# Kernel optimization log

Measured on AMD Instinct MI355X. Metric: run time of the kernel, lower is better.

## Reference

```python
import jax, jax.numpy as jnp
import numpy as np

N_HEAD = 16
N_STATE = 1024
D_HEAD = N_STATE // N_HEAD
B, T = 4, 2048


def setup_inputs() -> dict:
    key = jax.random.key(0)
    ks = jax.random.split(key, 9)
    x = jax.random.normal(ks[0], (B, T, N_STATE), dtype=jnp.float32)
    # causal additive mask, (T, T)
    neg = jnp.float32(-1e9)
    mask = jnp.where(jnp.tril(jnp.ones((T, T), dtype=bool)), 0.0, neg).astype(jnp.float32)
    s = 0.02  # keep activations in a sane range (module uses torch.randn init)
    Wq = jax.random.normal(ks[1], (N_STATE, N_STATE), dtype=jnp.float32) * s
    bq = jax.random.normal(ks[2], (N_STATE,), dtype=jnp.float32) * s
    Wk = jax.random.normal(ks[3], (N_STATE, N_STATE), dtype=jnp.float32) * s
    Wv = jax.random.normal(ks[4], (N_STATE, N_STATE), dtype=jnp.float32) * s
    bv = jax.random.normal(ks[5], (N_STATE,), dtype=jnp.float32) * s
    Wo = jax.random.normal(ks[6], (N_STATE, N_STATE), dtype=jnp.float32) * s
    bo = jax.random.normal(ks[7], (N_STATE,), dtype=jnp.float32) * s
    return {"x": x, "mask": mask, "Wq": Wq, "bq": bq, "Wk": Wk,
            "Wv": Wv, "bv": bv, "Wo": Wo, "bo": bo}


def reference(x, mask, Wq, bq, Wk, Wv, bv, Wo, bo):
    n, t, _ = x.shape
    scale = D_HEAD ** -0.25
    # projections: Linear stores weight as (out, in), applies x @ W.T
    q = x @ Wq.T + bq
    k = x @ Wk.T          # key has no bias
    v = x @ Wv.T + bv
    # (N, H, T, d)
    q = q.reshape(n, t, N_HEAD, D_HEAD).transpose(0, 2, 1, 3) * scale
    k = k.reshape(n, t, N_HEAD, D_HEAD).transpose(0, 2, 1, 3) * scale
    v = v.reshape(n, t, N_HEAD, D_HEAD).transpose(0, 2, 1, 3)
    qk = jnp.einsum('bhqd,bhkd->bhqk', q, k)
    qk = qk + mask[:t, :t]
    attn = jax.nn.softmax(qk, axis=-1)
    qkv = jnp.einsum('bhqk,bhkd->bhqd', attn, v)
    qkv = qkv.transpose(0, 2, 1, 3).reshape(n, t, N_STATE)
    return qkv @ Wo.T + bo
```

## Files before the change

kernel.cpp:

```cpp
#include <hip/hip_runtime.h>
#include <stdint.h>

#define DEVI __device__ __forceinline__

typedef float        f32x4   __attribute__((ext_vector_type(4)));
typedef float        f32x16  __attribute__((ext_vector_type(16)));
typedef __bf16       bf16x8  __attribute__((ext_vector_type(8)));
typedef unsigned short u16x8 __attribute__((ext_vector_type(8)));
typedef uint32_t     u32x2   __attribute__((ext_vector_type(2)));
typedef uint32_t     u32x4   __attribute__((ext_vector_type(4)));

static constexpr int TSEQ   = 2048;
static constexpr int NSTATE = 1024;
static constexpr int NHEAD  = 16;
static constexpr int DHEAD  = 64;
static constexpr int BATCH  = 4;
static constexpr int MROWS  = BATCH * TSEQ;
static constexpr float QSCALE = 0.125f * 1.44269504088896340736f;
static constexpr float DEFER_THR = 8.0f * 1.44269504088896340736f;

DEVI unsigned short f2bf(float f) {
  union { float f; uint32_t u; } v; v.f = f;
  return (unsigned short)((v.u + 0x7fffu + ((v.u >> 16) & 1u)) >> 16);
}

DEVI uint32_t cvt_pk_bf16(float lo, float hi) {
  uint32_t r;
  asm("v_cvt_pk_bf16_f32 %0, %1, %2" : "=v"(r) : "v"(lo), "v"(hi));
  return r;
}
DEVI float fexp2(float x) {
  float r;
  asm("v_exp_f32 %0, %1" : "=v"(r) : "v"(x));
  return r;
}

DEVI f32x4 mfma16(u16x8 a, u16x8 b, f32x4 c) {
  return __builtin_amdgcn_mfma_f32_16x16x32_bf16(
      __builtin_bit_cast(bf16x8, a), __builtin_bit_cast(bf16x8, b), c, 0, 0, 0);
}
DEVI f32x16 mfma32(u16x8 a, u16x8 b, f32x16 c) {
  return __builtin_amdgcn_mfma_f32_32x32x16_bf16(
      __builtin_bit_cast(bf16x8, a), __builtin_bit_cast(bf16x8, b), c, 0, 0, 0);
}

DEVI void gload_lds16(const void* g, void* l) {
  __builtin_amdgcn_global_load_lds(
      (const __attribute__((address_space(1))) void*)g,
      (__attribute__((address_space(3))) void*)l, 16, 0, 0);
}

__global__ void cvt_all(const float* __restrict__ x,
                        const float* __restrict__ w0, const float* __restrict__ w1,
                        const float* __restrict__ w2, const float* __restrict__ w3,
                        unsigned short* __restrict__ xb,
                        unsigned short* __restrict__ wb)
{
  const int NX = (MROWS * NSTATE) / 4;
  const int NW = (NSTATE * NSTATE) / 4;
  const int total = NX + 4 * NW;
  int i = blockIdx.x * blockDim.x + threadIdx.x;
  const int stride = gridDim.x * blockDim.x;
  for (; i < total; i += stride) {
    const float* src;
    unsigned short* dst;
    int j;
    if (i < NX) { src = x; dst = xb; j = i; }
    else {
      const int k = i - NX, wi = k >> 18;
      src = (wi == 0) ? w0 : (wi == 1) ? w1 : (wi == 2) ? w2 : w3;
      dst = wb + ((size_t)wi << 20);
      j = k & (NW - 1);
    }
    const float4 f = ((const float4*)src)[j];
    ushort4 o;
    o.x = f2bf(f.x); o.y = f2bf(f.y); o.z = f2bf(f.z); o.w = f2bf(f.w);
    ((ushort4*)dst)[j] = o;
  }
}

__global__ __launch_bounds__(256)
void gemm_qkv(const unsigned short* __restrict__ A,
              const unsigned short* __restrict__ Wqkv,
              const float* __restrict__ bq, const float* __restrict__ bv,
              unsigned short* __restrict__ Oqkv)
{
  __shared__ __align__(16) unsigned short As[128 * 32];
  __shared__ __align__(16) unsigned short Bs[128 * 32];
  const int t  = threadIdx.x;
  const int l  = t & 63, w = t >> 6;
  const int fr = l & 15, fq = l >> 4;
  const int wi = blockIdx.x >> 3;
  const int n0 = (blockIdx.x & 7) * 128;
  const int m0 = blockIdx.y * 128;
  const int wm = (w & 1) * 64, wn = (w >> 1) * 64;
  const unsigned short* Bw = Wqkv + ((size_t)wi << 20);
  unsigned short* Cq = Oqkv + ((size_t)wi << 23);

  f32x4 acc[4][4] = {};

  const int sr = t >> 2;
  const int sc = (t & 3) * 8;
  const unsigned short* ag = A  + (size_t)(m0 + sr) * NSTATE + sc;
  const unsigned short* bg = Bw + (size_t)(n0 + sr) * NSTATE + sc;
  unsigned short* lA0 = As + t * 8;
  unsigned short* lA1 = As + 2048 + t * 8;
  unsigned short* lB0 = Bs + t * 8;
  unsigned short* lB1 = Bs + 2048 + t * 8;

  for (int kt = 0; kt < NSTATE / 32; ++kt) {
    const int ko = kt * 32;
    gload_lds16(ag + ko,               lA0);
    gload_lds16(ag + 64 * NSTATE + ko, lA1);
    gload_lds16(bg + ko,               lB0);
    gload_lds16(bg + 64 * NSTATE + ko, lB1);
    __syncthreads();

    u16x8 a[4], b[4];
    #pragma unroll
    for (int i = 0; i < 4; ++i)
      a[i] = *(const u16x8*)(As + (wm + i * 16 + fr) * 32 + fq * 8);
    #pragma unroll
    for (int j = 0; j < 4; ++j)
      b[j] = *(const u16x8*)(Bs + (wn + j * 16 + fr) * 32 + fq * 8);
    #pragma unroll
    for (int i = 0; i < 4; ++i)
      #pragma unroll
      for (int j = 0; j < 4; ++j)
        acc[i][j] = mfma16(a[i], b[j], acc[i][j]);
    __syncthreads();
  }

  const int h = (n0 + wn) >> 6;
  #pragma unroll
  for (int j = 0; j < 4; ++j) {
    const int d = j * 16 + fr;
    const float bj = (wi == 1) ? 0.0f
                   : ((wi == 0) ? bq[n0 + wn + d] : bv[n0 + wn + d]);
    #pragma unroll
    for (int i = 0; i < 4; ++i) {
      #pragma unroll
      for (int r = 0; r < 4; ++r) {
        const int row = m0 + wm + i * 16 + fq * 4 + r;
        const int bb = row >> 11, tt = row & (TSEQ - 1);
        float v = acc[i][j][r] + bj;
        if (wi == 0) v *= QSCALE;
        Cq[(((size_t)(bb * NHEAD + h)) * TSEQ + tt) * DHEAD + d] = f2bf(v);
      }
    }
  }
}

__global__ __launch_bounds__(256)
void gemm_out(const unsigned short* __restrict__ A,
              const unsigned short* __restrict__ Bw,
              const float* __restrict__ bias,
              float* __restrict__ Co)
{
  __shared__ __align__(16) unsigned short As[128 * 32];
  __shared__ __align__(16) unsigned short Bs[128 * 32];
  const int t  = threadIdx.x;
  const int l  = t & 63, w = t >> 6;
  const int fr = l & 15, fq = l >> 4;
  const int m0 = blockIdx.y * 128, n0 = blockIdx.x * 128;
  const int wm = (w & 1) * 64, wn = (w >> 1) * 64;

  f32x4 acc[4][4] = {};

  const int sr = t >> 2;
  const int sc = (t & 3) * 8;
  const unsigned short* ag = A  + (size_t)(m0 + sr) * NSTATE + sc;
  const unsigned short* bg = Bw + (size_t)(n0 + sr) * NSTATE + sc;
  unsigned short* lA0 = As + t * 8;
  unsigned short* lA1 = As + 2048 + t * 8;
  unsigned short* lB0 = Bs + t * 8;
  unsigned short* lB1 = Bs + 2048 + t * 8;

  for (int kt = 0; kt < NSTATE / 32; ++kt) {
    const int ko = kt * 32;
    gload_lds16(ag + ko,               lA0);
    gload_lds16(ag + 64 * NSTATE + ko, lA1);
    gload_lds16(bg + ko,               lB0);
    gload_lds16(bg + 64 * NSTATE + ko, lB1);
    __syncthreads();

    u16x8 a[4], b[4];
    #pragma unroll
    for (int i = 0; i < 4; ++i)
      a[i] = *(const u16x8*)(As + (wm + i * 16 + fr) * 32 + fq * 8);
    #pragma unroll
    for (int j = 0; j < 4; ++j)
      b[j] = *(const u16x8*)(Bs + (wn + j * 16 + fr) * 32 + fq * 8);
    #pragma unroll
    for (int i = 0; i < 4; ++i)
      #pragma unroll
      for (int j = 0; j < 4; ++j)
        acc[i][j] = mfma16(a[i], b[j], acc[i][j]);
    __syncthreads();
  }

  #pragma unroll
  for (int j = 0; j < 4; ++j) {
    const int col = n0 + wn + j * 16 + fr;
    const float bj = bias[col];
    #pragma unroll
    for (int i = 0; i < 4; ++i) {
      const int row0 = m0 + wm + i * 16 + fq * 4;
      #pragma unroll
      for (int r = 0; r < 4; ++r)
        Co[(size_t)(row0 + r) * NSTATE + col] = acc[i][j][r] + bj;
    }
  }
}

__global__ __launch_bounds__(256)
void flash_attn(const unsigned short* __restrict__ Qg,
                const unsigned short* __restrict__ Kg,
                const unsigned short* __restrict__ Vg,
                unsigned short* __restrict__ O)
{
  const int bh = blockIdx.x;
  const int qb = 15 - (int)blockIdx.y;
  const int b  = bh >> 4, h = bh & 15;
  const int t  = threadIdx.x, lane = t & 63, w = t >> 6;
  const int lq = lane & 31, hi = lane >> 5;
  const size_t hoff = (size_t)bh * TSEQ * DHEAD;
  const unsigned short* Qp = Qg + hoff;
  const unsigned short* Kp = Kg + hoff;
  const unsigned short* Vp = Vg + hoff;

  __shared__ __align__(16) unsigned short Kb[2][64 * 64];
  __shared__ __align__(16) unsigned short Vb[2][64 * 64];

  const int qw   = qb * 128 + w * 32;
  const int qrow = qw + lq;

  u16x8 qf[4];
  #pragma unroll
  for (int c = 0; c < 4; ++c)
    qf[c] = *(const u16x8*)(Qp + (size_t)qrow * DHEAD + c * 16 + hi * 8);

  f32x16 oacc[2] = {};
  float m_r = -1e30f, l_r = 0.0f;

  const char* KbB = (const char*)&Kb[0][0];
  const char* VbB = (const char*)&Vb[0][0];
  int koff[4], voff[4];
  #pragma unroll
  for (int c = 0; c < 4; ++c) {
    koff[c] = lq * 128 + (((2 * c + hi) ^ (lane & 7)) << 4);
    voff[c] = lq * 128 + (((2 * c + hi) ^ (lq & 7)) << 4);
  }

  const int skr = t >> 2, skg = t & 3;
  const int svk2 = (t & 31) * 2;
  const int svd  = (t >> 5) * 8;

  const int nt = (qb + 1) * 2;

  #define STAGE_V(buf, va, vb)                                              \
    do {                                                                    \
      const u32x4 vau = __builtin_bit_cast(u32x4, va);                      \
      const u32x4 vbu = __builtin_bit_cast(u32x4, vb);                      \
      _Pragma("unroll")                                                     \
      for (int j = 0; j < 4; ++j) {                                         \
        const uint32_t pe = __builtin_amdgcn_perm(vbu[j], vau[j], 0x05040100); \
        const uint32_t po = __builtin_amdgcn_perm(vbu[j], vau[j], 0x07060302); \
        *(uint32_t*)(&Vb[buf][(svd + 2 * j) * 64 + (svk2 ^ ((2 * j) << 3))]) = pe; \
        *(uint32_t*)(&Vb[buf][(svd + 2 * j + 1) * 64 + (svk2 ^ ((2 * j + 1) << 3))]) = po; \
      }                                                                     \
    } while (0)

  {
    const u16x8 kr0 = *(const u16x8*)(Kp + (size_t)skr * DHEAD + skg * 16);
    const u16x8 kr1 = *(const u16x8*)(Kp + (size_t)skr * DHEAD + skg * 16 + 8);
    const u16x8 va  = *(const u16x8*)(Vp + (size_t)svk2 * DHEAD + svd);
    const u16x8 vb  = *(const u16x8*)(Vp + (size_t)(svk2 + 1) * DHEAD + svd);
    *(u16x8*)(&Kb[0][skr * 64 + (((skg * 2)     ^ (skr & 7)) << 3)]) = kr0;
    *(u16x8*)(&Kb[0][skr * 64 + (((skg * 2 + 1) ^ (skr & 7)) << 3)]) = kr1;
    STAGE_V(0, va, vb);
  }
  __syncthreads();

  for (int kt = 0; kt < nt; ++kt) {
    const int k0 = kt * 64;
    const int curB = (kt & 1) << 13;
    const bool pre = (kt + 1 < nt);
    u16x8 krn0, krn1, van, vbn;
    if (pre) {
      const int k0n = k0 + 64;
      krn0 = *(const u16x8*)(Kp + (size_t)(k0n + skr) * DHEAD + skg * 16);
      krn1 = *(const u16x8*)(Kp + (size_t)(k0n + skr) * DHEAD + skg * 16 + 8);
      van  = *(const u16x8*)(Vp + (size_t)(k0n + svk2) * DHEAD + svd);
      vbn  = *(const u16x8*)(Vp + (size_t)(k0n + svk2 + 1) * DHEAD + svd);
    }

    if (k0 < qw + 32) {
      f32x16 s[2];
      __builtin_amdgcn_s_setprio(1);
      #pragma unroll
      for (int t32 = 0; t32 < 2; ++t32) {
        if (k0 + t32 * 32 < qw + 32) {
          f32x16 z = {};
          #pragma unroll
          for (int c = 0; c < 4; ++c) {
            const u16x8 kf = *(const u16x8*)(KbB + curB + koff[c] + t32 * 4096);
            z = mfma32(kf, qf[c], z);
          }
          s[t32] = z;
        } else {
          #pragma unroll
          for (int r = 0; r < 16; ++r) s[t32][r] = -1e30f;
        }
      }
      __builtin_amdgcn_s_setprio(0);
      if (k0 + 63 > qw) {
        #pragma unroll
        for (int t32 = 0; t32 < 2; ++t32)
          #pragma unroll
          for (int r = 0; r < 16; ++r) {
            const int kk = k0 + t32 * 32 + (r & 3) + 8 * (r >> 2) + 4 * hi;
            if (kk > qrow) s[t32][r] = -1e30f;
          }
      }

      float mx = fmaxf(s[0][14], s[0][15]);
      #pragma unroll
      for (int r = 0; r < 14; r += 2) mx = fmaxf(fmaxf(mx, s[0][r]), s[0][r + 1]);
      #pragma unroll
      for (int r = 0; r < 16; r += 2) mx = fmaxf(fmaxf(mx, s[1][r]), s[1][r + 1]);
      mx = fmaxf(mx, __shfl_xor(mx, 32));

      if (__any(mx > m_r + DEFER_THR)) {
        const float mnew = fmaxf(m_r, mx);
        const float corr = fexp2(m_r - mnew);
        #pragma unroll
        for (int ds = 0; ds < 2; ++ds)
          #pragma unroll
          for (int r = 0; r < 16; ++r) oacc[ds][r] *= corr;
        l_r *= corr;
        m_r = mnew;
      }

      float ps = 0.0f;
      uint32_t pk[2][8];
      #pragma unroll
      for (int t32 = 0; t32 < 2; ++t32)
        #pragma unroll
        for (int m2 = 0; m2 < 8; ++m2) {
          const float pa = fexp2(s[t32][2 * m2]     - m_r);
          const float pb = fexp2(s[t32][2 * m2 + 1] - m_r);
          ps += pa + pb;
          pk[t32][m2] = cvt_pk_bf16(pa, pb);
        }
      ps += __shfl_xor(ps, 32);
      l_r += ps;

      uint32_t pf[2][2][4];
      #pragma unroll
      for (int t32 = 0; t32 < 2; ++t32)
        #pragma unroll
        for (int hf = 0; hf < 2; ++hf) {
          const u32x2 r02 = __builtin_amdgcn_permlane32_swap(
              pk[t32][hf * 4 + 0], pk[t32][hf * 4 + 2], false, false);
          const u32x2 r13 = __builtin_amdgcn_permlane32_swap(
              pk[t32][hf * 4 + 1], pk[t32][hf * 4 + 3], false, false);
          pf[t32][hf][0] = r02.x; pf[t32][hf][2] = r02.y;
          pf[t32][hf][1] = r13.x; pf[t32][hf][3] = r13.y;
        }

      __builtin_amdgcn_s_setprio(1);
      #pragma unroll
      for (int c = 0; c < 4; ++c) {
        if (k0 + 16 * c < qw + 32) {
          const u32x4 pw = {pf[c >> 1][c & 1][0], pf[c >> 1][c & 1][1],
                            pf[c >> 1][c & 1][2], pf[c >> 1][c & 1][3]};
          const u16x8 pv = __builtin_bit_cast(u16x8, pw);
          #pragma unroll
          for (int ds = 0; ds < 2; ++ds) {
            const u16x8 vf = *(const u16x8*)(VbB + curB + voff[c] + ds * 4096);
            oacc[ds] = mfma32(vf, pv, oacc[ds]);
          }
        }
      }
      __builtin_amdgcn_s_setprio(0);
    }

    if (pre) {
      const int nb = (kt & 1) ^ 1;
      *(u16x8*)(&Kb[nb][skr * 64 + (((skg * 2)     ^ (skr & 7)) << 3)]) = krn0;
      *(u16x8*)(&Kb[nb][skr * 64 + (((skg * 2 + 1) ^ (skr & 7)) << 3)]) = krn1;
      STAGE_V(nb, van, vbn);
    }
    __syncthreads();
  }

  const float inv = 1.0f / l_r;
  const size_t base = ((size_t)(b * TSEQ + qrow)) * NSTATE + h * DHEAD;
  #pragma unroll
  for (int ds = 0; ds < 2; ++ds)
    #pragma unroll
    for (int m2 = 0; m2 < 8; ++m2) {
      const int d = ds * 32 + 2 * (m2 & 1) + 8 * (m2 >> 1) + 4 * hi;
      *(uint32_t*)(O + base + d) =
          cvt_pk_bf16(oacc[ds][2 * m2] * inv, oacc[ds][2 * m2 + 1] * inv);
    }
  #undef STAGE_V
}

extern "C" void kernel_launch(void* const* d_in, const int* in_sizes, int n_in,
                              void* d_out, int out_size, void* d_ws, size_t ws_size,
                              hipStream_t stream)
{
  (void)in_sizes; (void)n_in; (void)out_size; (void)ws_size;
  const float* x  = (const float*)d_in[0];
  const float* Wq = (const float*)d_in[2];
  const float* bq = (const float*)d_in[3];
  const float* Wk = (const float*)d_in[4];
  const float* Wv = (const float*)d_in[5];
  const float* bv = (const float*)d_in[6];
  const float* Wo = (const float*)d_in[7];
  const float* bo = (const float*)d_in[8];

  char* ws = (char*)d_ws;
  unsigned short* xb  = (unsigned short*)(ws);
  unsigned short* wqb = (unsigned short*)(ws + (16u << 20));
  unsigned short* wob = wqb + (3u << 20);
  unsigned short* qb_ = (unsigned short*)(ws + (24u << 20));
  unsigned short* kb_ = (unsigned short*)(ws + (40u << 20));
  unsigned short* vb_ = (unsigned short*)(ws + (56u << 20));

  cvt_all<<<2048, 256, 0, stream>>>(x, Wq, Wk, Wv, Wo, xb, wqb);

  gemm_qkv<<<dim3(24, MROWS / 128), 256, 0, stream>>>(xb, wqb, bq, bv, qb_);

  flash_attn<<<dim3(BATCH * NHEAD, 16), 256, 0, stream>>>(qb_, kb_, vb_, xb);

  gemm_out<<<dim3(NSTATE / 128, MROWS / 128), 256, 0, stream>>>(xb, wob, bo, (float*)d_out);
}
```

Measured before the change: 186.2 us.

## Replace projection GEMMs with triple-buffered 256x128 tile kernel using swizzled LDS

Both the QKV and output projection GEMMs now use one templated kernel. It has 512 threads, a 256x128 tile, a K-step of 64 and a three-stage LDS ring buffer. Global-to-LDS loads are issued two stages ahead, with explicit vmcnt waits and a single barrier per iteration, and LDS rows use an XOR swizzle to avoid bank conflicts. MFMA issue is raised in priority with setprio. The aim is to hide global memory latency and halve the barriers per K of the old single-buffered 128x128 kernels, at the cost of much larger LDS use (about 144 KB per block), which limits occupancy, and fewer blocks in the grid.

```diff
diff --git a/kernel.cpp b/kernel.cpp
--- a/kernel.cpp
+++ b/kernel.cpp
@@ -79,136 +79,136 @@
   }
 }
 
-__global__ __launch_bounds__(256)
-void gemm_qkv(const unsigned short* __restrict__ A,
-              const unsigned short* __restrict__ Wqkv,
-              const float* __restrict__ bq, const float* __restrict__ bv,
-              unsigned short* __restrict__ Oqkv)
+template<int MODE>
+__global__ __launch_bounds__(512)
+void gemm_deep(const unsigned short* __restrict__ A,
+               const unsigned short* __restrict__ Wall,
+               const float* __restrict__ bq, const float* __restrict__ bv,
+               void* __restrict__ out)
 {
-  __shared__ __align__(16) unsigned short As[128 * 32];
-  __shared__ __align__(16) unsigned short Bs[128 * 32];
-  const int t  = threadIdx.x;
-  const int l  = t & 63, w = t >> 6;
-  const int fr = l & 15, fq = l >> 4;
-  const int wi = blockIdx.x >> 3;
-  const int n0 = (blockIdx.x & 7) * 128;
-  const int m0 = blockIdx.y * 128;
-  const int wm = (w & 1) * 64, wn = (w >> 1) * 64;
-  const unsigned short* Bw = Wqkv + ((size_t)wi << 20);
-  unsigned short* Cq = Oqkv + ((size_t)wi << 23);
+  constexpr int ASZ = 256 * 64;
+  constexpr int BSZ = 128 * 64;
+  constexpr int NT  = NSTATE / 64;
+  __shared__ __align__(16) unsigned short As[3 * ASZ];
+  __shared__ __align__(16) unsigned short Bs[3 * BSZ];
+
+  const int t = threadIdx.x, lane = t & 63, wid = t >> 6;
+  const int fr = lane & 15, fq = lane >> 4;
+  const int wm = wid >> 1, wn = wid & 1;
+  int wi, n0;
+  if (MODE == 0) { wi = blockIdx.x >> 3; n0 = (blockIdx.x & 7) * 128; }
+  else           { wi = 0;               n0 = blockIdx.x * 128; }
+  const int m0 = blockIdx.y * 256;
+  const unsigned short* Bw = Wall + ((size_t)wi << 20);
 
   f32x4 acc[4][4] = {};
 
-  const int sr = t >> 2;
-  const int sc = (t & 3) * 8;
-  const unsigned short* ag = A  + (size_t)(m0 + sr) * NSTATE + sc;
-  const unsigned short* bg = Bw + (size_t)(n0 + sr) * NSTATE + sc;
-  unsigned short* lA0 = As + t * 8;
-  unsigned short* lA1 = As + 2048 + t * 8;
-  unsigned short* lB0 = Bs + t * 8;
-  unsigned short* lB1 = Bs + 2048 + t * 8;
-
-  for (int kt = 0; kt < NSTATE / 32; ++kt) {
-    const int ko = kt * 32;
-    gload_lds16(ag + ko,               lA0);
-    gload_lds16(ag + 64 * NSTATE + ko, lA1);
-    gload_lds16(bg + ko,               lB0);
-    gload_lds16(bg + 64 * NSTATE + ko, lB1);
-    __syncthreads();
-
-    u16x8 a[4], b[4];
-    #pragma unroll
-    for (int i = 0; i < 4; ++i)
-      a[i] = *(const u16x8*)(As + (wm + i * 16 + fr) * 32 + fq * 8);
-    #pragma unroll
-    for (int j = 0; j < 4; ++j)
-      b[j] = *(const u16x8*)(Bs + (wn + j * 16 + fr) * 32 + fq * 8);
-    #pragma unroll
-    for (int i = 0; i < 4; ++i)
-      #pragma unroll
-      for (int j = 0; j < 4; ++j)
-        acc[i][j] = mfma16(a[i], b[j], acc[i][j]);
-    __syncthreads();
-  }
-
-  const int h = (n0 + wn) >> 6;
-  #pragma unroll
-  for (int j = 0; j < 4; ++j) {
-    const int d = j * 16 + fr;
-    const float bj = (wi == 1) ? 0.0f
-                   : ((wi == 0) ? bq[n0 + wn + d] : bv[n0 + wn + d]);
+  const int sg = (t & 7) ^ ((t >> 3) & 7);
+  const unsigned short* asrc[4];
+  const unsigned short* bsrc[2];
+  #pragma unroll
+  for (int q = 0; q < 4; ++q)
+    asrc[q] = A + (size_t)(m0 + q * 64 + (t >> 3)) * NSTATE + sg * 8;
+  #pragma unroll
+  for (int q = 0; q < 2; ++q)
+    bsrc[q] = Bw + (size_t)(n0 + q * 64 + (t >> 3)) * NSTATE + sg * 8;
+  const int ldst = t * 8;
+
+  int aofs[2][4], bofs[2][4];
+  #pragma unroll
+  for (int kk = 0; kk < 2; ++kk)
     #pragma unroll
     for (int i = 0; i < 4; ++i) {
-      #pragma unroll
-      for (int r = 0; r < 4; ++r) {
-        const int row = m0 + wm + i * 16 + fq * 4 + r;
-        const int bb = row >> 11, tt = row & (TSEQ - 1);
-        float v = acc[i][j][r] + bj;
-        if (wi == 0) v *= QSCALE;
-        Cq[(((size_t)(bb * NHEAD + h)) * TSEQ + tt) * DHEAD + d] = f2bf(v);
-      }
-    }
-  }
-}
-
-__global__ __launch_bounds__(256)
-void gemm_out(const unsigned short* __restrict__ A,
-              const unsigned short* __restrict__ Bw,
-              const float* __restrict__ bias,
-              float* __restrict__ Co)
-{
-  __shared__ __align__(16) unsigned short As[128 * 32];
-  __shared__ __align__(16) unsigned short Bs[128 * 32];
-  const int t  = threadIdx.x;
-  const int l  = t & 63, w = t >> 6;
-  const int fr = l & 15, fq = l >> 4;
-  const int m0 = blockIdx.y * 128, n0 = blockIdx.x * 128;
-  const int wm = (w & 1) * 64, wn = (w >> 1) * 64;
-
-  f32x4 acc[4][4] = {};
-
-  const int sr = t >> 2;
-  const int sc = (t & 3) * 8;
-  const unsigned short* ag = A  + (size_t)(m0 + sr) * NSTATE + sc;
-  const unsigned short* bg = Bw + (size_t)(n0 + sr) * NSTATE + sc;
-  unsigned short* lA0 = As + t * 8;
-  unsigned short* lA1 = As + 2048 + t * 8;
-  unsigned short* lB0 = Bs + t * 8;
-  unsigned short* lB1 = Bs + 2048 + t * 8;
-
-  for (int kt = 0; kt < NSTATE / 32; ++kt) {
-    const int ko = kt * 32;
-    gload_lds16(ag + ko,               lA0);
-    gload_lds16(ag + 64 * NSTATE + ko, lA1);
-    gload_lds16(bg + ko,               lB0);
-    gload_lds16(bg + 64 * NSTATE + ko, lB1);
-    __syncthreads();
-
-    u16x8 a[4], b[4];
+      const int sl = ((kk * 4 + fq) ^ (fr & 7)) * 8;
+      aofs[kk][i] = (wm * 64 + i * 16 + fr) * 64 + sl;
+      bofs[kk][i] = (wn * 64 + i * 16 + fr) * 64 + sl;
+    }
+
+  #define STAGE(nb, kt)                                              \
+    do {                                                             \
+      unsigned short* ab_ = As + (nb) * ASZ;                         \
+      unsigned short* bb_ = Bs + (nb) * BSZ;                         \
+      _Pragma("unroll")                                              \
+      for (int q = 0; q < 4; ++q)                                    \
+        gload_lds16(asrc[q] + (kt) * 64, ab_ + q * 4096 + ldst);     \
+      _Pragma("unroll")                                              \
+      for (int q = 0; q < 2; ++q)                                    \
+        gload_lds16(bsrc[q] + (kt) * 64, bb_ + q * 4096 + ldst);     \
+    } while (0)
+
+  STAGE(0, 0);
+  STAGE(1, 1);
+  asm volatile("s_waitcnt vmcnt(6)" ::: "memory");
+  __builtin_amdgcn_sched_barrier(0);
+  __builtin_amdgcn_s_barrier();
+  __builtin_amdgcn_sched_barrier(0);
+
+  int cur = 0;
+  for (int kt = 0; kt < NT; ++kt) {
+    const unsigned short* ab = As + cur * ASZ;
+    const unsigned short* bb = Bs + cur * BSZ;
+    const bool pre = (kt + 2) < NT;
+    int nb = cur + 2; if (nb >= 3) nb -= 3;
+    if (pre) STAGE(nb, kt + 2);
+
     #pragma unroll
-    for (int i = 0; i < 4; ++i)
-      a[i] = *(const u16x8*)(As + (wm + i * 16 + fr) * 32 + fq * 8);
+    for (int kk = 0; kk < 2; ++kk) {
+      u16x8 af[4], bf[4];
+      #pragma unroll
+      for (int i = 0; i < 4; ++i) af[i] = *(const u16x8*)(ab + aofs[kk][i]);
+      #pragma unroll
+      for (int i = 0; i < 4; ++i) bf[i] = *(const u16x8*)(bb + bofs[kk][i]);
+      __builtin_amdgcn_s_setprio(1);
+      #pragma unroll
+      for (int i = 0; i < 4; ++i)
+        #pragma unroll
+        for (int j = 0; j < 4; ++j)
+          acc[i][j] = mfma16(af[i], bf[j], acc[i][j]);
+      __builtin_amdgcn_s_setprio(0);
+    }
+
+    if (pre) asm volatile("s_waitcnt vmcnt(6)" ::: "memory");
+    else     asm volatile("s_waitcnt vmcnt(0)" ::: "memory");
+    __builtin_amdgcn_sched_barrier(0);
+    __builtin_amdgcn_s_barrier();
+    __builtin_amdgcn_sched_barrier(0);
+    cur += 1; if (cur == 3) cur = 0;
+  }
+  #undef STAGE
+
+  if (MODE == 0) {
+    unsigned short* Cq = (unsigned short*)out + ((size_t)wi << 23);
+    const int h = (n0 >> 6) + wn;
     #pragma unroll
-    for (int j = 0; j < 4; ++j)
-      b[j] = *(const u16x8*)(Bs + (wn + j * 16 + fr) * 32 + fq * 8);
+    for (int j = 0; j < 4; ++j) {
+      const int d = j * 16 + fr;
+      const int ncol = n0 + wn * 64 + d;
+      const float bj = (wi == 1) ? 0.0f : ((wi == 0) ? bq[ncol] : bv[ncol]);
+      #pragma unroll
+      for (int i = 0; i < 4; ++i) {
+        #pragma unroll
+        for (int r = 0; r < 4; ++r) {
+          const int row = m0 + wm * 64 + i * 16 + fq * 4 + r;
+          const int bb_ = row >> 11, tt = row & (TSEQ - 1);
+          float v = acc[i][j][r] + bj;
+          if (wi == 0) v *= QSCALE;
+          Cq[(((size_t)(bb_ * NHEAD + h)) * TSEQ + tt) * DHEAD + d] = f2bf(v);
+        }
+      }
+    }
+  } else {
+    float* Co = (float*)out;
     #pragma unroll
-    for (int i = 0; i < 4; ++i)
-      #pragma unroll
-      for (int j = 0; j < 4; ++j)
-        acc[i][j] = mfma16(a[i], b[j], acc[i][j]);
-    __syncthreads();
-  }
-
-  #pragma unroll
-  for (int j = 0; j < 4; ++j) {
-    const int col = n0 + wn + j * 16 + fr;
-    const float bj = bias[col];
-    #pragma unroll
-    for (int i = 0; i < 4; ++i) {
-      const int row0 = m0 + wm + i * 16 + fq * 4;
-      #pragma unroll
-      for (int r = 0; r < 4; ++r)
-        Co[(size_t)(row0 + r) * NSTATE + col] = acc[i][j][r] + bj;
+    for (int j = 0; j < 4; ++j) {
+      const int col = n0 + wn * 64 + j * 16 + fr;
+      const float bj = bq[col];
+      #pragma unroll
+      for (int i = 0; i < 4; ++i) {
+        const int row0 = m0 + wm * 64 + i * 16 + fq * 4;
+        #pragma unroll
+        for (int r = 0; r < 4; ++r)
+          Co[(size_t)(row0 + r) * NSTATE + col] = acc[i][j][r] + bj;
+      }
     }
   }
 }
@@ -432,9 +432,9 @@
 
   cvt_all<<<2048, 256, 0, stream>>>(x, Wq, Wk, Wv, Wo, xb, wqb);
 
-  gemm_qkv<<<dim3(24, MROWS / 128), 256, 0, stream>>>(xb, wqb, bq, bv, qb_);
+  gemm_deep<0><<<dim3(24, MROWS / 256), 512, 0, stream>>>(xb, wqb, bq, bv, qb_);
 
   flash_attn<<<dim3(BATCH * NHEAD, 16), 256, 0, stream>>>(qb_, kb_, vb_, xb);
 
-  gemm_out<<<dim3(NSTATE / 128, MROWS / 128), 256, 0, stream>>>(xb, wob, bo, (float*)d_out);
-}
+  gemm_deep<1><<<dim3(NSTATE / 128, MROWS / 256), 512, 0, stream>>>(xb, wob, bo, nullptr, d_out);
+}
```

Result: slower. 192.7 us (+3.5%).
